# Kernel optimization log

Measured on AMD Instinct MI355X. Metric: run time of the kernel, lower is better.

## Reference

```python
import jax, jax.numpy as jnp
import numpy as np

N = 100000        # nodes
E = 1600000       # edges
D = 32            # hidden dim
C = 2             # num classes
NL = 4            # layer_num - 1 GIN layers
G = 512           # graphs in batch
BN_EPS = 1e-3     # keras BatchNormalization default epsilon


def setup_inputs() -> dict:
    key = jax.random.key(0)
    ks = jax.random.split(key, 16)
    s = 0.1
    return {
        "node_embeddings": jax.random.normal(ks[0], (N, D), dtype=jnp.float32),
        "edge_index": jax.random.randint(ks[1], (2, E), 0, N, dtype=jnp.int32),
        "batch": jnp.sort(jax.random.randint(ks[2], (N,), 0, G, dtype=jnp.int32)),
        # MLP inner dense + BN (per GIN layer)
        "W1": jax.random.normal(ks[3], (NL, D, D), dtype=jnp.float32) * s,
        "b1": jnp.zeros((NL, D), jnp.float32),
        "bn1_g": jnp.ones((NL, D), jnp.float32),
        "bn1_b": jnp.zeros((NL, D), jnp.float32),
        # MLP output dense
        "W2": jax.random.normal(ks[4], (NL, D, D), dtype=jnp.float32) * s,
        "b2": jnp.zeros((NL, D), jnp.float32),
        # ApplyNodeFunc BN
        "bn2_g": jnp.ones((NL, D), jnp.float32),
        "bn2_b": jnp.zeros((NL, D), jnp.float32),
        # outer per-layer BN
        "norm_g": jnp.ones((NL, D), jnp.float32),
        "norm_b": jnp.zeros((NL, D), jnp.float32),
        # readout heads: one Dense(num_classes) per hidden_rep level (layer_num of them)
        "dense_W": jax.random.normal(ks[5], (NL + 1, D, C), dtype=jnp.float32) * s,
        "dense_b": jnp.zeros((NL + 1, C), jnp.float32),
    }


def _bn(x, g, b):
    # inference-mode BatchNorm with init moving stats (mean=0, var=1)
    return x * (g / jnp.sqrt(1.0 + BN_EPS)) + b


def reference(node_embeddings, edge_index, batch, W1, b1, bn1_g, bn1_b,
              W2, b2, bn2_g, bn2_b, norm_g, norm_b, dense_W, dense_b):
    src, dst = edge_index[0], edge_index[1]
    h = node_embeddings
    hidden = [h]
    for i in range(NL):
        # GIN aggregation: (1+eps)*h + sum of neighbor features (eps=0)
        agg = jax.ops.segment_sum(h[src], dst, num_segments=N)  # [N, D]
        z = h + agg
        # ApplyNodeFunc: MLP (Dense->BN->ReLU->Dense) then BN + ReLU
        z = jax.nn.relu(_bn(z @ W1[i] + b1[i], bn1_g[i], bn1_b[i]))
        z = z @ W2[i] + b2[i]
        z = jax.nn.relu(_bn(z, bn2_g[i], bn2_b[i]))
        # outer norm + relu
        h = jax.nn.relu(_bn(z, norm_g[i], norm_b[i]))
        hidden.append(h)
    # readout: segment-sum pooling per hidden level, Dense(num_classes), summed
    score = jnp.zeros((G, C), dtype=node_embeddings.dtype)
    for i, hr in enumerate(hidden):
        pool = jax.ops.segment_sum(hr, batch, num_segments=G)  # [G, D]
        score = score + pool @ dense_W[i] + dense_b[i]
    return jax.nn.softmax(score, axis=-1)
```

## Files before the change

### kernel.cpp

```cpp
#include <hip/hip_runtime.h>

#define NN 100000
#define EE 1600000
#define DD 32
#define CC 2
#define NLAYERS 4
#define GG 512

#define BSH 9
#define BW 512
#define NBUK ((NN + BW - 1) / BW)
#define CAP 12288
#define CH 2048
#define NPART ((EE + CH - 1) / CH)

__global__ void part_kernel(const int* __restrict__ ei,
                            int* __restrict__ gcur,
                            unsigned* __restrict__ part) {
    __shared__ unsigned sorted[CH];
    __shared__ unsigned char sbkt[CH];
    __shared__ int cnt[NBUK], offs[NBUK], cur[NBUK], gbs[NBUK];

    const int tid = threadIdx.x;
    const int eb  = blockIdx.x * CH;
    const int nch = min(CH, EE - eb);

    for (int b = tid; b < NBUK; b += 256) cnt[b] = 0;
    __syncthreads();
    for (int i = tid; i < nch; i += 256) {
        int dn = ei[EE + eb + i];
        atomicAdd(&cnt[dn >> BSH], 1);
    }
    __syncthreads();
    if (tid == 0) {
        int o = 0;
        for (int b = 0; b < NBUK; ++b) { offs[b] = o; o += cnt[b]; }
    }
    __syncthreads();
    if (tid < NBUK) {
        cur[tid] = offs[tid];
        gbs[tid] = cnt[tid] ? atomicAdd(&gcur[tid], cnt[tid]) : 0;
    }
    __syncthreads();
    for (int i = tid; i < nch; i += 256) {
        int s  = ei[eb + i];
        int dn = ei[EE + eb + i];
        int b  = dn >> BSH;
        unsigned pk = ((unsigned)(dn & (BW - 1)) << 17) | (unsigned)s;
        int p = atomicAdd(&cur[b], 1);
        sorted[p] = pk;
        sbkt[p]   = (unsigned char)b;
    }
    __syncthreads();
    for (int i = tid; i < nch; i += 256) {
        int b = sbkt[i];
        part[(size_t)b * CAP + gbs[b] + (i - offs[b])] = sorted[i];
    }
}

__global__ void bscan_kernel(const int* __restrict__ gcur,
                             int* __restrict__ bbase,
                             int* __restrict__ row_ptr) {
    if (threadIdx.x == 0 && blockIdx.x == 0) {
        int o = 0;
        for (int b = 0; b < NBUK; ++b) { bbase[b] = o; o += gcur[b]; }
        row_ptr[NN] = EE;
    }
}

__global__ void lcsr_kernel(const unsigned* __restrict__ part,
                            const int* __restrict__ gcur,
                            const int* __restrict__ bbase,
                            int* __restrict__ row_ptr,
                            int* __restrict__ csr_src) {
    __shared__ int hcnt[BW];
    __shared__ int a[2][BW];
    __shared__ int ccur[BW];
    const int t    = threadIdx.x;
    const int b    = blockIdx.x;
    const int cntb = gcur[b];
    const int base = bbase[b];
    const size_t pb = (size_t)b * CAP;

    hcnt[t] = 0;
    __syncthreads();
    for (int i = t; i < cntb; i += BW)
        atomicAdd(&hcnt[part[pb + i] >> 17], 1);
    __syncthreads();
    int x = hcnt[t];
    a[0][t] = x;
    __syncthreads();
    int cb = 0;
    for (int off = 1; off < BW; off <<= 1) {
        int v = a[cb][t];
        if (t >= off) v += a[cb][t - off];
        a[cb ^ 1][t] = v;
        cb ^= 1;
        __syncthreads();
    }
    const int excl = a[cb][t] - x;
    const int node = b * BW + t;
    if (node < NN) row_ptr[node] = base + excl;
    ccur[t] = excl;
    __syncthreads();
    for (int i = t; i < cntb; i += BW) {
        unsigned pk = part[pb + i];
        int dl  = pk >> 17;
        int pos = base + atomicAdd(&ccur[dl], 1);
        csr_src[pos] = (int)(pk & 0x1FFFFu);
    }
}

__global__ __launch_bounds__(256) void layer_kernel(
    const float* __restrict__ h_in, float* __restrict__ h_out,
    const int* __restrict__ row_ptr, const int* __restrict__ csr_src,
    const int* __restrict__ batch,
    const float* __restrict__ W1, const float* __restrict__ b1,
    const float* __restrict__ g1, const float* __restrict__ bt1,
    const float* __restrict__ W2, const float* __restrict__ b2,
    const float* __restrict__ g2, const float* __restrict__ bt2,
    const float* __restrict__ ng, const float* __restrict__ nb,
    const float* __restrict__ dWl, float* __restrict__ score) {
    __shared__ float sp[8 * DD];
    __shared__ float sdW[DD * CC];
    __shared__ float ss[GG * CC];
    __shared__ float zA[64][DD];
    __shared__ float z2loc[8][DD];

    const int tid = threadIdx.x;
    const int j = tid >> 5;
    const int d = tid & 31;

    float w1r[DD], w2r[DD];
    #pragma unroll
    for (int k = 0; k < DD; ++k) w1r[k] = W1[k * DD + d];
    #pragma unroll
    for (int k = 0; k < DD; ++k) w2r[k] = W2[k * DD + d];

    if (tid < DD) {
        sp[0 * DD + tid] = b1[tid];
        sp[1 * DD + tid] = g1[tid];
        sp[2 * DD + tid] = bt1[tid];
        sp[3 * DD + tid] = b2[tid];
        sp[4 * DD + tid] = g2[tid];
        sp[5 * DD + tid] = bt2[tid];
        sp[6 * DD + tid] = ng[tid];
        sp[7 * DD + tid] = nb[tid];
    }
    if (tid < DD * CC) sdW[tid] = dWl[tid];
    for (int i = tid; i < GG * CC; i += 256) ss[i] = 0.f;

    const float invs = 1.0f / sqrtf(1.001f);
    const int base = blockIdx.x * 64;

    for (int s = 0; s < 8; ++s) {
        const int local = j * 8 + s;
        const int n = base + local;
        if (n < NN) {
            float acc = h_in[(size_t)n * DD + d];
            int e = row_ptr[n];
            const int e1 = row_ptr[n + 1];
            for (; e + 8 <= e1; e += 8) {
                int i0 = csr_src[e + 0], i1 = csr_src[e + 1];
                int i2 = csr_src[e + 2], i3 = csr_src[e + 3];
                int i4 = csr_src[e + 4], i5 = csr_src[e + 5];
                int i6 = csr_src[e + 6], i7 = csr_src[e + 7];
                float v0 = h_in[(size_t)i0 * DD + d];
                float v1 = h_in[(size_t)i1 * DD + d];
                float v2 = h_in[(size_t)i2 * DD + d];
                float v3 = h_in[(size_t)i3 * DD + d];
                float v4 = h_in[(size_t)i4 * DD + d];
                float v5 = h_in[(size_t)i5 * DD + d];
                float v6 = h_in[(size_t)i6 * DD + d];
                float v7 = h_in[(size_t)i7 * DD + d];
                acc += ((v0 + v1) + (v2 + v3)) + ((v4 + v5) + (v6 + v7));
            }
            for (; e < e1; ++e)
                acc += h_in[(size_t)csr_src[e] * DD + d];
            zA[local][d] = acc;
        }
    }
    __syncthreads();

    for (int s = 0; s < 8; ++s) {
        const int local = j * 8 + s;
        const int n = base + local;
        if (n >= NN) break;

        float a1 = sp[0 * DD + d];
        #pragma unroll
        for (int kk = 0; kk < DD; kk += 4) {
            const float4 zv = *reinterpret_cast<const float4*>(&zA[local][kk]);
            a1 += zv.x * w1r[kk] + zv.y * w1r[kk + 1] +
                  zv.z * w1r[kk + 2] + zv.w * w1r[kk + 3];
        }
        float v = fmaxf(a1 * (sp[1 * DD + d] * invs) + sp[2 * DD + d], 0.f);
        z2loc[j][d] = v;

        float a2 = sp[3 * DD + d];
        #pragma unroll
        for (int kk = 0; kk < DD; kk += 4) {
            const float4 zv = *reinterpret_cast<const float4*>(&z2loc[j][kk]);
            a2 += zv.x * w2r[kk] + zv.y * w2r[kk + 1] +
                  zv.z * w2r[kk + 2] + zv.w * w2r[kk + 3];
        }
        float w = fmaxf(a2 * (sp[4 * DD + d] * invs) + sp[5 * DD + d], 0.f);
        w = fmaxf(w * (sp[6 * DD + d] * invs) + sp[7 * DD + d], 0.f);
        h_out[(size_t)n * DD + d] = w;

        float p0 = w * sdW[d * CC + 0];
        float p1 = w * sdW[d * CC + 1];
        #pragma unroll
        for (int off = 16; off > 0; off >>= 1) {
            p0 += __shfl_xor(p0, off, 32);
            p1 += __shfl_xor(p1, off, 32);
        }
        if (d == 0) {
            int g = batch[n];
            atomicAdd(&ss[g * CC + 0], p0);
            atomicAdd(&ss[g * CC + 1], p1);
        }
    }
    __syncthreads();

    for (int i = tid; i < GG * CC; i += 256) {
        float v = ss[i];
        if (v != 0.f) atomicAdd(&score[i], v);
    }
}

__global__ void pool_kernel(const float* __restrict__ h,
                            const int* __restrict__ batch,
                            const float* __restrict__ Wd,
                            float* __restrict__ score) {
    __shared__ float ss[GG * CC];
    __shared__ float sW[DD * CC];
    const int tid = threadIdx.x;
    for (int i = tid; i < GG * CC; i += 256) ss[i] = 0.f;
    if (tid < DD * CC) sW[tid] = Wd[tid];
    __syncthreads();

    const int d = tid & 31;
    const int grp = tid >> 5;
    const int n0 = blockIdx.x * 512;
    const int n1 = (n0 + 512 < NN) ? (n0 + 512) : NN;

    for (int n = n0 + grp; n < n1; n += 8) {
        float v = h[(size_t)n * DD + d];
        float p0 = v * sW[d * CC + 0];
        float p1 = v * sW[d * CC + 1];
        #pragma unroll
        for (int off = 16; off > 0; off >>= 1) {
            p0 += __shfl_xor(p0, off, 32);
            p1 += __shfl_xor(p1, off, 32);
        }
        if (d == 0) {
            int g = batch[n];
            atomicAdd(&ss[g * CC + 0], p0);
            atomicAdd(&ss[g * CC + 1], p1);
        }
    }
    __syncthreads();

    for (int i = tid; i < GG * CC; i += 256) {
        float v = ss[i];
        if (v != 0.f) atomicAdd(&score[i], v);
    }
}

__global__ void softmax_kernel(const float* __restrict__ score,
                               const float* __restrict__ db,
                               float* __restrict__ out) {
    int g = blockIdx.x * blockDim.x + threadIdx.x;
    if (g >= GG) return;
    float bs0 = 0.f, bs1 = 0.f;
    #pragma unroll
    for (int i = 0; i <= NLAYERS; ++i) {
        bs0 += db[i * CC + 0];
        bs1 += db[i * CC + 1];
    }
    float s0 = score[g * CC + 0] + bs0;
    float s1 = score[g * CC + 1] + bs1;
    float m = fmaxf(s0, s1);
    float e0 = expf(s0 - m), e1 = expf(s1 - m);
    float inv = 1.f / (e0 + e1);
    out[g * CC + 0] = e0 * inv;
    out[g * CC + 1] = e1 * inv;
}

extern "C" void kernel_launch(void* const* d_in, const int* in_sizes, int n_in,
                              void* d_out, int out_size, void* d_ws, size_t ws_size,
                              hipStream_t stream) {
    (void)in_sizes; (void)n_in; (void)out_size; (void)ws_size;

    const float* node_emb = (const float*)d_in[0];
    const int*   ei       = (const int*)d_in[1];
    const int*   batch    = (const int*)d_in[2];
    const float* W1       = (const float*)d_in[3];
    const float* b1       = (const float*)d_in[4];
    const float* g1       = (const float*)d_in[5];
    const float* bt1      = (const float*)d_in[6];
    const float* W2       = (const float*)d_in[7];
    const float* b2       = (const float*)d_in[8];
    const float* g2       = (const float*)d_in[9];
    const float* bt2      = (const float*)d_in[10];
    const float* ng       = (const float*)d_in[11];
    const float* nb       = (const float*)d_in[12];
    const float* dW       = (const float*)d_in[13];
    const float* db       = (const float*)d_in[14];
    float* out = (float*)d_out;

    float* hA      = (float*)d_ws;
    float* hB      = hA + (size_t)NN * DD;
    unsigned* part = (unsigned*)hB;
    float* score   = hB + (size_t)NN * DD;
    int* row_ptr   = (int*)(score + GG * CC);
    int* csr_src   = row_ptr + NN + 2;
    int* gcur      = csr_src + EE;
    int* bbase     = gcur + 256;

    hipMemsetAsync(gcur, 0, 256 * sizeof(int), stream);
    hipMemsetAsync(score, 0, GG * CC * sizeof(float), stream);

    part_kernel<<<NPART, 256, 0, stream>>>(ei, gcur, part);
    bscan_kernel<<<1, 64, 0, stream>>>(gcur, bbase, row_ptr);
    lcsr_kernel<<<NBUK, BW, 0, stream>>>(part, gcur, bbase, row_ptr, csr_src);

    pool_kernel<<<(NN + 511) / 512, 256, 0, stream>>>(node_emb, batch, dW, score);

    const int layerGrid = (NN + 63) / 64;
    const float* cur_in = node_emb;
    float* bufs[2] = {hA, hB};
    for (int i = 0; i < NLAYERS; ++i) {
        float* o = bufs[i & 1];
        layer_kernel<<<layerGrid, 256, 0, stream>>>(
            cur_in, o, row_ptr, csr_src, batch,
            W1 + (size_t)i * DD * DD, b1 + i * DD, g1 + i * DD, bt1 + i * DD,
            W2 + (size_t)i * DD * DD, b2 + i * DD, g2 + i * DD, bt2 + i * DD,
            ng + i * DD, nb + i * DD,
            dW + (size_t)(i + 1) * DD * CC, score);
        cur_in = o;
    }

    softmax_kernel<<<(GG + 255) / 256, 256, 0, stream>>>(score, db, out);
}
```

Before: 472.2 us.

## Balance gather across warps with edge-parallel chunks and LDS atomics

Each block's neighbour aggregation changes from one warp walking whole node rows to an even split of the block's contiguous edge range across its 8 warps. Each edge's local destination is stored in a new byte array built during CSR construction, and contributions are summed into shared memory with atomic adds, using 16 loads in flight per thread. This targets load imbalance from skewed degrees and aims for more memory-level parallelism. In exchange it adds one extra byte read per edge, LDS atomic traffic, a different float summation order, and a launch-bounds occupancy hint that may cap registers.

```diff
diff --git a/kernel.cpp b/kernel.cpp
--- a/kernel.cpp
+++ b/kernel.cpp
@@ -72,7 +72,8 @@
                             const int* __restrict__ gcur,
                             const int* __restrict__ bbase,
                             int* __restrict__ row_ptr,
-                            int* __restrict__ csr_src) {
+                            int* __restrict__ csr_src,
+                            unsigned char* __restrict__ csr_dl) {
     __shared__ int hcnt[BW];
     __shared__ int a[2][BW];
     __shared__ int ccur[BW];
@@ -108,12 +109,14 @@
         int dl  = pk >> 17;
         int pos = base + atomicAdd(&ccur[dl], 1);
         csr_src[pos] = (int)(pk & 0x1FFFFu);
-    }
-}
-
-__global__ __launch_bounds__(256) void layer_kernel(
+        csr_dl[pos]  = (unsigned char)(dl & 63);
+    }
+}
+
+__global__ __launch_bounds__(256, 4) void layer_kernel(
     const float* __restrict__ h_in, float* __restrict__ h_out,
     const int* __restrict__ row_ptr, const int* __restrict__ csr_src,
+    const unsigned char* __restrict__ csr_dl,
     const int* __restrict__ batch,
     const float* __restrict__ W1, const float* __restrict__ b1,
     const float* __restrict__ g1, const float* __restrict__ bt1,
@@ -153,32 +156,41 @@
     const float invs = 1.0f / sqrtf(1.001f);
     const int base = blockIdx.x * 64;
 
+    #pragma unroll
     for (int s = 0; s < 8; ++s) {
         const int local = j * 8 + s;
         const int n = base + local;
-        if (n < NN) {
-            float acc = h_in[(size_t)n * DD + d];
-            int e = row_ptr[n];
-            const int e1 = row_ptr[n + 1];
-            for (; e + 8 <= e1; e += 8) {
-                int i0 = csr_src[e + 0], i1 = csr_src[e + 1];
-                int i2 = csr_src[e + 2], i3 = csr_src[e + 3];
-                int i4 = csr_src[e + 4], i5 = csr_src[e + 5];
-                int i6 = csr_src[e + 6], i7 = csr_src[e + 7];
-                float v0 = h_in[(size_t)i0 * DD + d];
-                float v1 = h_in[(size_t)i1 * DD + d];
-                float v2 = h_in[(size_t)i2 * DD + d];
-                float v3 = h_in[(size_t)i3 * DD + d];
-                float v4 = h_in[(size_t)i4 * DD + d];
-                float v5 = h_in[(size_t)i5 * DD + d];
-                float v6 = h_in[(size_t)i6 * DD + d];
-                float v7 = h_in[(size_t)i7 * DD + d];
-                acc += ((v0 + v1) + (v2 + v3)) + ((v4 + v5) + (v6 + v7));
-            }
-            for (; e < e1; ++e)
-                acc += h_in[(size_t)csr_src[e] * DD + d];
-            zA[local][d] = acc;
-        }
+        zA[local][d] = (n < NN) ? h_in[(size_t)n * DD + d] : 0.f;
+    }
+    __syncthreads();
+
+    {
+        const int nEnd = (base + 64 < NN) ? (base + 64) : NN;
+        const int E0 = row_ptr[base];
+        const int E1 = row_ptr[nEnd];
+        const int cnt = E1 - E0;
+        const int chunk = (cnt + 7) >> 3;
+        int g0 = E0 + j * chunk;
+        int g1 = g0 + chunk;
+        if (g0 > E1) g0 = E1;
+        if (g1 > E1) g1 = E1;
+
+        int e = g0;
+        for (; e + 16 <= g1; e += 16) {
+            int idx[16];
+            #pragma unroll
+            for (int i = 0; i < 16; ++i) idx[i] = csr_src[e + i];
+            int dl[16];
+            #pragma unroll
+            for (int i = 0; i < 16; ++i) dl[i] = csr_dl[e + i];
+            float v[16];
+            #pragma unroll
+            for (int i = 0; i < 16; ++i) v[i] = h_in[(size_t)idx[i] * DD + d];
+            #pragma unroll
+            for (int i = 0; i < 16; ++i) atomicAdd(&zA[dl[i]][d], v[i]);
+        }
+        for (; e < g1; ++e)
+            atomicAdd(&zA[csr_dl[e]][d], h_in[(size_t)csr_src[e] * DD + d]);
     }
     __syncthreads();
 
@@ -318,13 +330,14 @@
     int* csr_src   = row_ptr + NN + 2;
     int* gcur      = csr_src + EE;
     int* bbase     = gcur + 256;
+    unsigned char* csr_dl = (unsigned char*)(bbase + 256);
 
     hipMemsetAsync(gcur, 0, 256 * sizeof(int), stream);
     hipMemsetAsync(score, 0, GG * CC * sizeof(float), stream);
 
     part_kernel<<<NPART, 256, 0, stream>>>(ei, gcur, part);
     bscan_kernel<<<1, 64, 0, stream>>>(gcur, bbase, row_ptr);
-    lcsr_kernel<<<NBUK, BW, 0, stream>>>(part, gcur, bbase, row_ptr, csr_src);
+    lcsr_kernel<<<NBUK, BW, 0, stream>>>(part, gcur, bbase, row_ptr, csr_src, csr_dl);
 
     pool_kernel<<<(NN + 511) / 512, 256, 0, stream>>>(node_emb, batch, dW, score);
 
@@ -334,7 +347,7 @@
     for (int i = 0; i < NLAYERS; ++i) {
         float* o = bufs[i & 1];
         layer_kernel<<<layerGrid, 256, 0, stream>>>(
-            cur_in, o, row_ptr, csr_src, batch,
+            cur_in, o, row_ptr, csr_src, csr_dl, batch,
             W1 + (size_t)i * DD * DD, b1 + i * DD, g1 + i * DD, bt1 + i * DD,
             W2 + (size_t)i * DD * DD, b2 + i * DD, g2 + i * DD, bt2 + i * DD,
             ng + i * DD, nb + i * DD,
```

Result: slower. 1.403 ms (+197.0%).
